# Kernel tuning notes

Hardware: AMD Instinct MI355X
Metric: run time of the kernel (lower is better)

## Reference

```python
import jax, jax.numpy as jnp
import numpy as np

VOCAB, EMB, H, TRK, L, BOUND = 50257, 1024, 1024, 1024, 256, 25

def setup_inputs() -> dict:
    key = jax.random.key(0)
    ks = jax.random.split(key, 16)
    s = 0.02
    return {
        "query_words": jax.random.normal(ks[0], (L, 1, H), jnp.float32),
        "query_vector": jax.random.normal(ks[1], (1, 1, TRK), jnp.float32),
        "decision_vector": jax.random.normal(ks[2], (1, 1, H), jnp.float32),
        "target_answer": jax.random.randint(ks[3], (BOUND, 1, 1), 0, VOCAB, jnp.int64),
        "emb_table": jax.random.normal(ks[4], (VOCAB, EMB), jnp.float32) * s,
        "gru_Wih": jax.random.normal(ks[5], (3 * H, EMB + TRK), jnp.float32) * s,
        "gru_Whh": jax.random.normal(ks[6], (3 * H, H), jnp.float32) * s,
        "gru_bih": jnp.zeros((3 * H,), jnp.float32),
        "gru_bhh": jnp.zeros((3 * H,), jnp.float32),
        "attn_Wq": jax.random.normal(ks[7], (H, H), jnp.float32) * s,
        "attn_bq": jnp.zeros((H,), jnp.float32),
        "attn_Wk": jax.random.normal(ks[8], (H, H), jnp.float32) * s,
        "attn_bk": jnp.zeros((H,), jnp.float32),
        "attn_v": jax.random.normal(ks[9], (H,), jnp.float32) * s,
        "concat_W": jax.random.normal(ks[10], (H, 2 * H), jnp.float32) * s,
        "concat_b": jnp.zeros((H,), jnp.float32),
        "out_W": jax.random.normal(ks[11], (VOCAB, H), jnp.float32) * s,
        "out_b": jnp.zeros((VOCAB,), jnp.float32),
    }


def reference(query_words, query_vector, decision_vector, target_answer,
              emb_table, gru_Wih, gru_Whh, gru_bih, gru_bhh,
              attn_Wq, attn_bq, attn_Wk, attn_bk, attn_v,
              concat_W, concat_b, out_W, out_b):
    # eval-mode: dropout = identity; tf_ratio=1 -> teacher forcing for all steps
    h_dim = decision_vector.shape[-1]
    qw = query_words[:, 0, :]                      # [L, H] encoder memory
    keys = qw @ attn_Wk.T + attn_bk                # precompute key projection once
    qv = query_vector.reshape(-1)                  # [TRK]
    h0 = decision_vector.reshape(-1)               # [H]
    ta = target_answer.reshape(-1).astype(jnp.int32)
    # input token per step: SOS (0), then teacher-forced targets
    idx_seq = jnp.concatenate([jnp.zeros((1,), jnp.int32), ta[: BOUND - 1]])

    def step(h, idx):
        x = jnp.concatenate([qv, emb_table[idx]])  # cat(query_vector, embedded)
        g = gru_Wih @ x + gru_bih                  # [3H]
        gh = gru_Whh @ h + gru_bhh                 # [3H]
        r = jax.nn.sigmoid(g[:h_dim] + gh[:h_dim])
        z = jax.nn.sigmoid(g[h_dim:2 * h_dim] + gh[h_dim:2 * h_dim])
        n = jnp.tanh(g[2 * h_dim:] + r * gh[2 * h_dim:])
        h_new = (1.0 - z) * n + z * h
        # additive (Bahdanau) attention over query_words
        e = jnp.tanh(keys + attn_Wq @ h_new + attn_bq) @ attn_v  # [L]
        w = jax.nn.softmax(e)
        ctx = w @ qw                                              # [H]
        vec = jnp.tanh(concat_W @ jnp.concatenate([h_new, ctx]) + concat_b)
        logits = out_W @ vec + out_b                              # [VOCAB]
        return h_new, jax.nn.log_softmax(logits)

    _, logps = jax.lax.scan(step, h0, idx_seq)     # [BOUND, VOCAB]
    answer = jnp.argmax(logps, axis=-1)            # greedy tokens per step
    return (answer, logps)
```

## Files before the change

### kernel.cpp

```cpp
#include <hip/hip_runtime.h>
#include <math.h>

#define VOCAB 50257
#define EMB 1024
#define HD 1024
#define TRK 1024
#define LQ 256
#define BND 25
#define SENT 0xAAAAAAAAu

__device__ __forceinline__ float wred(float s){
  #pragma unroll
  for (int m = 32; m >= 1; m >>= 1) s += __shfl_xor(s, m, 64);
  return s;
}

__global__ __launch_bounds__(256) void k_pre_keys(const float* __restrict__ Wih,
                                                  const float* __restrict__ qv,
                                                  const float* __restrict__ bih,
                                                  const int*   __restrict__ ta,
                                                  const float* __restrict__ emb,
                                                  const float* __restrict__ qw,
                                                  const float* __restrict__ Wk,
                                                  float* __restrict__ gib,
                                                  float* __restrict__ E,
                                                  float* __restrict__ part){
  __shared__ float qt[64*256];
  int b = blockIdx.x, tid = threadIdx.x;
  if (b < 768){
    int w = tid >> 6, lane = tid & 63;
    int row = b*4 + w;
    const float* a = Wih + (size_t)row*2048;
    float s = 0.f;
    #pragma unroll
    for (int e = 0; e < 4; e++){
      int k = e*256 + lane*4;
      float4 av = *(const float4*)(a + k);
      float4 qr = *(const float4*)(qv + k);
      s += av.x*qr.x + av.y*qr.y + av.z*qr.z + av.w*qr.w;
    }
    s = wred(s);
    if (lane == 0) gib[row] = s + bih[row];
    return;
  }
  if (b < 868){
    int g = (b - 768)*256 + tid;
    int t = g >> 10, i = g & 1023;
    int idx = (t == 0) ? 0 : ta[t-1];
    E[g] = emb[(size_t)idx*EMB + i];
    return;
  }
  int b2 = b - 868;
  int jb = b2 & 63;
  int ks = b2 >> 6;
  int l = tid;
  float acc[16];
  #pragma unroll
  for (int j = 0; j < 16; j++) acc[j] = 0.f;

  for (int kt = 0; kt < 4; kt++){
    int kb = ks*256 + kt*64;
    __syncthreads();
    #pragma unroll
    for (int p = 0; p < 16; p++){
      int fidx = (p*256 + tid)*4;
      int kk = fidx & 63, ll = fidx >> 6;
      float4 v = *(const float4*)(qw + (size_t)ll*1024 + kb + kk);
      qt[(kk+0)*256 + (ll ^ ((kk+0)&31))] = v.x;
      qt[(kk+1)*256 + (ll ^ ((kk+1)&31))] = v.y;
      qt[(kk+2)*256 + (ll ^ ((kk+2)&31))] = v.z;
      qt[(kk+3)*256 + (ll ^ ((kk+3)&31))] = v.w;
    }
    __syncthreads();
    #pragma unroll
    for (int s = 0; s < 4; s++){
      float qr[16];
      #pragma unroll
      for (int q = 0; q < 16; q++){
        int k = s*16 + q;
        qr[q] = qt[k*256 + (l ^ (k&31))];
      }
      #pragma unroll
      for (int j = 0; j < 16; j++){
        const float* wr = Wk + (size_t)(jb*16 + j)*1024 + kb + s*16;
        #pragma unroll
        for (int q4 = 0; q4 < 4; q4++){
          float4 wv = *(const float4*)(wr + q4*4);
          acc[j] += qr[q4*4+0]*wv.x + qr[q4*4+1]*wv.y
                  + qr[q4*4+2]*wv.z + qr[q4*4+3]*wv.w;
        }
      }
    }
  }
  #pragma unroll
  for (int j = 0; j < 16; j++)
    part[((size_t)ks*1024 + jb*16 + j)*256 + l] = acc[j];
}

template<int K, int NCH>
__global__ __launch_bounds__(256) void k_gemm_s2(const float* __restrict__ A, int lda,
                                                 const float* __restrict__ B, int ldb,
                                                 const float* __restrict__ bias,
                                                 float* __restrict__ C,
                                                 int R, int N, int act){
  __shared__ float Bl[NCH*K];
  constexpr int KD4 = K/4;
  int tid = threadIdx.x, w = tid >> 6, lane = tid & 63;
  int row = blockIdx.x*4 + w;
  const float* a = A + (size_t)row*lda;
  float4 ar[K/256];
  #pragma unroll
  for (int e = 0; e < K/256; e++)
    ar[e] = *(const float4*)(a + e*256 + lane*4);
  float bs = bias[row];
  for (int c0 = 0; c0 < N; c0 += NCH){
    int nt = min(NCH, N - c0);
    __syncthreads();
    int total = nt*KD4;
    for (int i = tid; i < total; i += 256){
      int j = i/KD4, kk = i - j*KD4;
      *(float4*)&Bl[j*K + kk*4] = *(const float4*)(B + (size_t)(c0+j)*ldb + kk*4);
    }
    __syncthreads();
    for (int j = 0; j < nt; j++){
      float s = 0.f;
      #pragma unroll
      for (int e = 0; e < K/256; e++){
        float4 bv = *(const float4*)&Bl[j*K + e*256 + lane*4];
        s += ar[e].x*bv.x + ar[e].y*bv.y + ar[e].z*bv.z + ar[e].w*bv.w;
      }
      s = wred(s);
      if (lane == 0){
        float v = s + bs;
        if (act) v = tanhf(v);
        C[(size_t)(c0+j)*R + row] = v;
      }
    }
  }
}

__global__ __launch_bounds__(512, 1) void k_gru8(const float* __restrict__ Whh,
                                                 const float* __restrict__ bhh,
                                                 const float* __restrict__ gi,
                                                 const float* __restrict__ dv,
                                                 float* __restrict__ HC,
                                                 unsigned* __restrict__ hxu){
  __shared__ float Wl[24][1024];
  __shared__ float hbuf[1024];
  __shared__ float sres[24];
  int tid = threadIdx.x, w = tid >> 6, lane = tid & 63;
  int b = blockIdx.x;
  for (int i = tid; i < 6144; i += 512){
    int r = i >> 8, c = (i & 255)*4;
    int g = r >> 3, s = r & 7;
    *(float4*)&Wl[r][c] = *(const float4*)(Whh + (size_t)(g*1024 + b*8 + s)*1024 + c);
  }
  if (tid < 256)
    *(float4*)&hbuf[tid*4] = *(const float4*)(dv + tid*4);
  __syncthreads();

  for (int t = 0; t < BND; t++){
    float g0=0,g1=0,g2=0,bb0=0,bb1=0,bb2=0,hpown=0;
    if (tid < 8){
      int i = b*8 + tid;
      const float* gg = gi + (size_t)t*3072;
      g0 = gg[i]; g1 = gg[1024+i]; g2 = gg[2048+i];
      bb0 = bhh[i]; bb1 = bhh[1024+i]; bb2 = bhh[2048+i];
      hpown = hbuf[i];
    }
    float hv[16];
    #pragma unroll
    for (int e = 0; e < 4; e++){
      float4 v = *(const float4*)&hbuf[e*256 + lane*4];
      hv[e*4]=v.x; hv[e*4+1]=v.y; hv[e*4+2]=v.z; hv[e*4+3]=v.w;
    }
    #pragma unroll
    for (int j = 0; j < 3; j++){
      int r = w*3 + j;
      float a = 0.f;
      #pragma unroll
      for (int e = 0; e < 4; e++){
        float4 v = *(const float4*)&Wl[r][e*256 + lane*4];
        a += v.x*hv[e*4] + v.y*hv[e*4+1] + v.z*hv[e*4+2] + v.w*hv[e*4+3];
      }
      a = wred(a);
      if (lane == 0) sres[r] = a;
    }
    __syncthreads();
    if (tid < 8){
      int i = b*8 + tid;
      float ghr = sres[tid]      + bb0;
      float ghz = sres[8  + tid] + bb1;
      float ghn = sres[16 + tid] + bb2;
      float rr = 1.f/(1.f + expf(-(g0 + ghr)));
      float zz = 1.f/(1.f + expf(-(g1 + ghz)));
      float nn = tanhf(g2 + rr*ghn);
      float hnew = (1.f - zz)*nn + zz*hpown;
      HC[(size_t)t*2048 + i] = hnew;
      if (t < BND-1){
        union { float f; unsigned u; } cv; cv.f = hnew;
        if (cv.u == SENT) cv.u ^= 1u;
        __hip_atomic_store(hxu + (size_t)t*2048 + b*16 + tid, cv.u,
                           __ATOMIC_RELAXED, __HIP_MEMORY_SCOPE_AGENT);
      }
    }
    if (t == BND-1) break;
    if (w < 2){
      int blk = w*64 + lane;
      const unsigned* bp = hxu + (size_t)t*2048 + blk*16;
      unsigned d[8];
      for (;;){
        bool ok = true;
        #pragma unroll
        for (int j = 0; j < 8; j++){
          d[j] = __hip_atomic_load(bp + j, __ATOMIC_RELAXED, __HIP_MEMORY_SCOPE_AGENT);
          ok = ok && (d[j] != SENT);
        }
        if (ok) break;
        __builtin_amdgcn_s_sleep(1);
      }
      #pragma unroll
      for (int j = 0; j < 8; j++)
        hbuf[blk*8 + j] = __uint_as_float(d[j]);
    }
    __syncthreads();
  }
}

__global__ __launch_bounds__(256) void k_attn1(const float* __restrict__ part,
                                               const float* __restrict__ bk,
                                               const float* __restrict__ Qt,
                                               const float* __restrict__ av,
                                               float* __restrict__ epart){
  int t = blockIdx.x, jc = blockIdx.y;
  int l = threadIdx.x;
  const float* q = Qt + (size_t)t*1024;
  int j0 = jc*32;
  float acc = 0.f;
  #pragma unroll
  for (int u = 0; u < 8; u++){
    #pragma unroll
    for (int v = 0; v < 4; v++){
      int j = j0 + u*4 + v;
      float kv = part[(size_t)j*256 + l]
               + part[(size_t)(1024+j)*256 + l]
               + part[(size_t)(2048+j)*256 + l]
               + part[(size_t)(3072+j)*256 + l]
               + bk[j];
      acc += tanhf(kv + q[j]) * av[j];
    }
  }
  epart[((size_t)t*32 + jc)*256 + l] = acc;
}

__global__ __launch_bounds__(256) void k_attn2(const float* __restrict__ epart,
                                               const float* __restrict__ qw,
                                               float* __restrict__ HC){
  __shared__ float red[256];
  __shared__ float sw[256];
  int t = blockIdx.x, tid = threadIdx.x;
  float e = 0.f;
  for (int jc = 0; jc < 32; jc++) e += epart[((size_t)t*32 + jc)*256 + tid];
  red[tid] = e; __syncthreads();
  for (int s = 128; s > 0; s >>= 1){
    if (tid < s) red[tid] = fmaxf(red[tid], red[tid+s]);
    __syncthreads();
  }
  float m = red[0]; __syncthreads();
  float wv = expf(e - m);
  red[tid] = wv; __syncthreads();
  for (int s = 128; s > 0; s >>= 1){
    if (tid < s) red[tid] += red[tid+s];
    __syncthreads();
  }
  float inv = 1.f/red[0];
  sw[tid] = wv*inv; __syncthreads();
  float4 c = make_float4(0.f,0.f,0.f,0.f);
  const float* qp = qw + tid*4;
  for (int ll = 0; ll < 256; ll++){
    float wl = sw[ll];
    float4 v = *(const float4*)(qp + (size_t)ll*1024);
    c.x += wl*v.x; c.y += wl*v.y; c.z += wl*v.z; c.w += wl*v.w;
  }
  *(float4*)(HC + (size_t)t*2048 + 1024 + tid*4) = c;
}

__global__ __launch_bounds__(256, 1) void k_gemm_big9(const float* __restrict__ A,
                                                      const float* __restrict__ B,
                                                      const float* __restrict__ bias,
                                                      float* __restrict__ C){
  __shared__ float Bl[25600];
  int tid = threadIdx.x;
  int rl = tid & 63;
  int q  = tid >> 6;
  int R0 = blockIdx.x*256;

  for (int i = tid; i < 6400; i += 256){
    int t = i >> 8, kk = (i & 255) << 2;
    *(float4*)&Bl[t*1024 + kk] = *(const float4*)(B + (size_t)t*1024 + kk);
  }

  const float* ap[4];
  #pragma unroll
  for (int j = 0; j < 4; j++){
    int r = R0 + 64*j + rl;
    if (r >= VOCAB) r = VOCAB-1;
    ap[j] = A + (size_t)r*1024 + q*256;
  }

  float acc[4][25];
  #pragma unroll
  for (int j = 0; j < 4; j++)
    #pragma unroll
    for (int t = 0; t < 25; t++) acc[j][t] = 0.f;

  float4 a[4][4];
  #pragma unroll
  for (int j = 0; j < 4; j++){
    a[j][0] = *(const float4*)(ap[j] + 0);
    a[j][1] = *(const float4*)(ap[j] + 4);
    a[j][2] = *(const float4*)(ap[j] + 8);
    a[j][3] = *(const float4*)(ap[j] + 12);
  }
  __syncthreads();

  const float* bq = Bl + q*256;
  #pragma unroll 1
  for (int kb = 0; kb < 256; kb += 16){
    float4 n[4][4];
    if (kb + 16 < 256){
      #pragma unroll
      for (int j = 0; j < 4; j++){
        n[j][0] = *(const float4*)(ap[j] + kb + 16);
        n[j][1] = *(const float4*)(ap[j] + kb + 20);
        n[j][2] = *(const float4*)(ap[j] + kb + 24);
        n[j][3] = *(const float4*)(ap[j] + kb + 28);
      }
    }
    #pragma unroll
    for (int t = 0; t < 25; t++){
      const float* bt = bq + t*1024 + kb;
      float4 b0 = *(const float4*)(bt + 0);
      float4 b1 = *(const float4*)(bt + 4);
      float4 b2 = *(const float4*)(bt + 8);
      float4 b3 = *(const float4*)(bt + 12);
      #pragma unroll
      for (int j = 0; j < 4; j++){
        acc[j][t] += a[j][0].x*b0.x + a[j][0].y*b0.y + a[j][0].z*b0.z + a[j][0].w*b0.w
                   + a[j][1].x*b1.x + a[j][1].y*b1.y + a[j][1].z*b1.z + a[j][1].w*b1.w
                   + a[j][2].x*b2.x + a[j][2].y*b2.y + a[j][2].z*b2.z + a[j][2].w*b2.w
                   + a[j][3].x*b3.x + a[j][3].y*b3.y + a[j][3].z*b3.z + a[j][3].w*b3.w;
      }
    }
    #pragma unroll
    for (int j = 0; j < 4; j++){
      a[j][0] = n[j][0]; a[j][1] = n[j][1]; a[j][2] = n[j][2]; a[j][3] = n[j][3];
    }
  }

  for (int tc0 = 0; tc0 < 25; tc0 += 13){
    int nt = min(13, 25 - tc0);
    __syncthreads();
    #pragma unroll
    for (int j = 0; j < 4; j++)
      for (int tt = 0; tt < nt; tt++)
        Bl[(q*256 + j*64 + rl)*13 + tt] = acc[j][tc0 + tt];
    __syncthreads();
    for (int v = tid; v < 256*nt; v += 256){
      int rr = v & 255, tt = v >> 8;
      float s = 0.f;
      #pragma unroll
      for (int qq = 0; qq < 4; qq++)
        s += Bl[(qq*256 + rr)*13 + tt];
      int row = R0 + rr;
      if (row < VOCAB)
        C[(size_t)(tc0 + tt)*VOCAB + row] = s + bias[row];
    }
  }
}

__global__ __launch_bounds__(256) void k_lstat(const float* __restrict__ C,
                                               float* __restrict__ pm,
                                               float* __restrict__ ps,
                                               int*   __restrict__ pa){
  __shared__ float sm[256], ss[256];
  __shared__ int   sa[256];
  int t = blockIdx.x, c = blockIdx.y, tid = threadIdx.x;
  int r0 = c*6283, r1 = min(r0 + 6283, VOCAB);
  const float* p = C + (size_t)t*VOCAB;
  float m = -3.4e38f, s = 0.f; int arg = r0;
  for (int r = r0 + tid; r < r1; r += 256){
    float x = p[r];
    if (x > m){ s = s*expf(m - x) + 1.f; m = x; arg = r; }
    else       s += expf(x - m);
  }
  sm[tid] = m; ss[tid] = s; sa[tid] = arg; __syncthreads();
  for (int st = 128; st > 0; st >>= 1){
    if (tid < st){
      float m1 = sm[tid], s1 = ss[tid]; int a1 = sa[tid];
      float m2 = sm[tid+st], s2 = ss[tid+st]; int a2 = sa[tid+st];
      if (m2 > m1){ sm[tid] = m2; ss[tid] = s2 + s1*expf(m1 - m2); sa[tid] = a2; }
      else if (m2 == m1){ ss[tid] = s1 + s2; sa[tid] = min(a1, a2); }
      else { ss[tid] = s1 + s2*expf(m2 - m1); }
    }
    __syncthreads();
  }
  if (tid == 0){ pm[t*8 + c] = sm[0]; ps[t*8 + c] = ss[0]; pa[t*8 + c] = sa[0]; }
}

__global__ __launch_bounds__(256) void k_lsub2(float* __restrict__ C,
                                               const float* __restrict__ pm,
                                               const float* __restrict__ ps,
                                               const int* __restrict__ pa,
                                               float* __restrict__ out){
  int t = blockIdx.y;
  float M = pm[t*8], S = ps[t*8]; int A = pa[t*8];
  #pragma unroll
  for (int c = 1; c < 8; c++){
    float m2 = pm[t*8+c], s2 = ps[t*8+c]; int a2 = pa[t*8+c];
    if (m2 > M){ S = s2 + S*expf(M - m2); M = m2; A = a2; }
    else if (m2 == M){ S += s2; A = min(A, a2); }
    else S += s2*expf(m2 - M);
  }
  float Lg = logf(S) + M;
  int r = blockIdx.x*256 + threadIdx.x;
  if (r < VOCAB) C[(size_t)t*VOCAB + r] -= Lg;
  if (blockIdx.x == 0 && threadIdx.x == 0) out[t] = (float)A;
}

extern "C" void kernel_launch(void* const* d_in, const int* in_sizes, int n_in,
                              void* d_out, int out_size, void* d_ws, size_t ws_size,
                              hipStream_t stream){
  const float* qw  = (const float*)d_in[0];
  const float* qv  = (const float*)d_in[1];
  const float* dv  = (const float*)d_in[2];
  const int*   ta  = (const int*)d_in[3];
  const float* emb = (const float*)d_in[4];
  const float* Wih = (const float*)d_in[5];
  const float* Whh = (const float*)d_in[6];
  const float* bih = (const float*)d_in[7];
  const float* bhh = (const float*)d_in[8];
  const float* Wq  = (const float*)d_in[9];
  const float* bq  = (const float*)d_in[10];
  const float* Wk  = (const float*)d_in[11];
  const float* bk  = (const float*)d_in[12];
  const float* av  = (const float*)d_in[13];
  const float* cW  = (const float*)d_in[14];
  const float* cb  = (const float*)d_in[15];
  const float* oW  = (const float*)d_in[16];
  const float* ob  = (const float*)d_in[17];
  float* out = (float*)d_out;
  float* ws  = (float*)d_ws;

  float* part  = ws;
  float* ep    = ws + 1048576;
  float* E     = ws + 1310720;
  float* gib   = ws + 1336320;
  float* gi    = ws + 1339392;
  float* HC    = ws + 1416192;
  float* Qt    = ws + 1467392;
  float* VEC   = ws + 1492992;
  unsigned* hx = (unsigned*)(ws + 1518592);
  float* pm    = ws + 1569792;
  float* ps    = ws + 1570048;
  int*   pa    = (int*)(ws + 1570304);

  hipMemsetAsync(hx, 0xAA, 51200*4, stream);
  k_pre_keys<<<1124, 256, 0, stream>>>(Wih, qv, bih, ta, emb, qw, Wk, gib, E, part);
  k_gemm_s2<1024,16><<<768, 256, 0, stream>>>(Wih + 1024, 2048, E, 1024, gib, gi, 3072, 25, 0);
  k_gru8<<<128, 512, 0, stream>>>(Whh, bhh, gi, dv, HC, hx);
  k_gemm_s2<1024,16><<<256, 256, 0, stream>>>(Wq, 1024, HC, 2048, bq, Qt, 1024, 25, 0);
  k_attn1<<<dim3(25,32), 256, 0, stream>>>(part, bk, Qt, av, ep);
  k_attn2<<<25, 256, 0, stream>>>(ep, qw, HC);
  k_gemm_s2<2048,8><<<256, 256, 0, stream>>>(cW, 2048, HC, 2048, cb, VEC, 1024, 25, 1);
  k_gemm_big9<<<197, 256, 0, stream>>>(oW, VEC, ob, out + 25);
  k_lstat<<<dim3(25,8), 256, 0, stream>>>(out + 25, pm, ps, pa);
  k_lsub2<<<dim3(197,25), 256, 0, stream>>>(out + 25, pm, ps, pa, out);
}
```

Baseline: 396.0 us.

## Compute output projection with split-bf16 MFMA instead of FP32 FMA

Replaces the FP32 FMA output-vocabulary GEMM with a matrix-core kernel. Both operands are split into bf16 high and low parts, and three MFMA products (hi*hi, hi*lo, lo*hi) approximate FP32 accuracy. A small new kernel pre-splits the 25 decoder vectors, while the weight rows are split on the fly in registers. The aim is to shorten the largest GEMM (50257x1024x25), at the cost of conversion ALU work, an extra launch and slightly reduced precision.

```diff
diff --git a/kernel.cpp b/kernel.cpp
--- a/kernel.cpp
+++ b/kernel.cpp
@@ -8,6 +8,9 @@
 #define LQ 256
 #define BND 25
 #define SENT 0xAAAAAAAAu
+
+typedef __attribute__((ext_vector_type(8))) short short8v;
+typedef __attribute__((ext_vector_type(4))) float float4v;
 
 __device__ __forceinline__ float wred(float s){
   #pragma unroll
@@ -285,96 +288,92 @@
   *(float4*)(HC + (size_t)t*2048 + 1024 + tid*4) = c;
 }
 
-__global__ __launch_bounds__(256, 1) void k_gemm_big9(const float* __restrict__ A,
-                                                      const float* __restrict__ B,
+__global__ __launch_bounds__(256) void k_bconv(const float* __restrict__ VEC,
+                                               short* __restrict__ Bhi,
+                                               short* __restrict__ Blo){
+  int i = blockIdx.x*256 + threadIdx.x;
+  if (i < 25600){
+    float v = VEC[i];
+    unsigned bits = __float_as_uint(v);
+    unsigned hib = bits & 0xFFFF0000u;
+    Bhi[i] = (short)(bits >> 16);
+    float lo = v - __uint_as_float(hib);
+    Blo[i] = (short)(__float_as_uint(lo) >> 16);
+  }
+}
+
+__global__ __launch_bounds__(256, 1) void k_gemm_mfma(const float* __restrict__ A,
+                                                      const short* __restrict__ Bhi,
+                                                      const short* __restrict__ Blo,
                                                       const float* __restrict__ bias,
                                                       float* __restrict__ C){
-  __shared__ float Bl[25600];
-  int tid = threadIdx.x;
-  int rl = tid & 63;
-  int q  = tid >> 6;
-  int R0 = blockIdx.x*256;
-
-  for (int i = tid; i < 6400; i += 256){
-    int t = i >> 8, kk = (i & 255) << 2;
-    *(float4*)&Bl[t*1024 + kk] = *(const float4*)(B + (size_t)t*1024 + kk);
-  }
+  int tid = threadIdx.x, lane = tid & 63, w = tid >> 6;
+  int rlo = lane & 15, kg = lane >> 4;
+  int R0 = blockIdx.x*256 + w*64;
 
   const float* ap[4];
   #pragma unroll
-  for (int j = 0; j < 4; j++){
-    int r = R0 + 64*j + rl;
-    if (r >= VOCAB) r = VOCAB-1;
-    ap[j] = A + (size_t)r*1024 + q*256;
-  }
-
-  float acc[4][25];
-  #pragma unroll
-  for (int j = 0; j < 4; j++)
-    #pragma unroll
-    for (int t = 0; t < 25; t++) acc[j][t] = 0.f;
-
-  float4 a[4][4];
-  #pragma unroll
-  for (int j = 0; j < 4; j++){
-    a[j][0] = *(const float4*)(ap[j] + 0);
-    a[j][1] = *(const float4*)(ap[j] + 4);
-    a[j][2] = *(const float4*)(ap[j] + 8);
-    a[j][3] = *(const float4*)(ap[j] + 12);
-  }
-  __syncthreads();
-
-  const float* bq = Bl + q*256;
+  for (int rt = 0; rt < 4; rt++){
+    int row = R0 + rt*16 + rlo;
+    if (row >= VOCAB) row = VOCAB-1;
+    ap[rt] = A + (size_t)row*1024 + kg*8;
+  }
+  int t0 = rlo;
+  int t1 = 16 + rlo; if (t1 > 24) t1 = 24;
+  const short* bh0 = Bhi + t0*1024 + kg*8;
+  const short* bl0 = Blo + t0*1024 + kg*8;
+  const short* bh1 = Bhi + t1*1024 + kg*8;
+  const short* bl1 = Blo + t1*1024 + kg*8;
+
+  float4v acc[4][2];
+  #pragma unroll
+  for (int rt = 0; rt < 4; rt++)
+    #pragma unroll
+    for (int ct = 0; ct < 2; ct++)
+      acc[rt][ct] = (float4v){0.f,0.f,0.f,0.f};
+
   #pragma unroll 1
-  for (int kb = 0; kb < 256; kb += 16){
-    float4 n[4][4];
-    if (kb + 16 < 256){
-      #pragma unroll
-      for (int j = 0; j < 4; j++){
-        n[j][0] = *(const float4*)(ap[j] + kb + 16);
-        n[j][1] = *(const float4*)(ap[j] + kb + 20);
-        n[j][2] = *(const float4*)(ap[j] + kb + 24);
-        n[j][3] = *(const float4*)(ap[j] + kb + 28);
-      }
-    }
-    #pragma unroll
-    for (int t = 0; t < 25; t++){
-      const float* bt = bq + t*1024 + kb;
-      float4 b0 = *(const float4*)(bt + 0);
-      float4 b1 = *(const float4*)(bt + 4);
-      float4 b2 = *(const float4*)(bt + 8);
-      float4 b3 = *(const float4*)(bt + 12);
-      #pragma unroll
-      for (int j = 0; j < 4; j++){
-        acc[j][t] += a[j][0].x*b0.x + a[j][0].y*b0.y + a[j][0].z*b0.z + a[j][0].w*b0.w
-                   + a[j][1].x*b1.x + a[j][1].y*b1.y + a[j][1].z*b1.z + a[j][1].w*b1.w
-                   + a[j][2].x*b2.x + a[j][2].y*b2.y + a[j][2].z*b2.z + a[j][2].w*b2.w
-                   + a[j][3].x*b3.x + a[j][3].y*b3.y + a[j][3].z*b3.z + a[j][3].w*b3.w;
-      }
-    }
-    #pragma unroll
-    for (int j = 0; j < 4; j++){
-      a[j][0] = n[j][0]; a[j][1] = n[j][1]; a[j][2] = n[j][2]; a[j][3] = n[j][3];
-    }
-  }
-
-  for (int tc0 = 0; tc0 < 25; tc0 += 13){
-    int nt = min(13, 25 - tc0);
-    __syncthreads();
-    #pragma unroll
-    for (int j = 0; j < 4; j++)
-      for (int tt = 0; tt < nt; tt++)
-        Bl[(q*256 + j*64 + rl)*13 + tt] = acc[j][tc0 + tt];
-    __syncthreads();
-    for (int v = tid; v < 256*nt; v += 256){
-      int rr = v & 255, tt = v >> 8;
-      float s = 0.f;
-      #pragma unroll
-      for (int qq = 0; qq < 4; qq++)
-        s += Bl[(qq*256 + rr)*13 + tt];
-      int row = R0 + rr;
-      if (row < VOCAB)
-        C[(size_t)(tc0 + tt)*VOCAB + row] = s + bias[row];
+  for (int s = 0; s < 32; s++){
+    int ko = s*32;
+    short8v bh[2], bl[2];
+    bh[0] = *(const short8v*)(bh0 + ko);
+    bl[0] = *(const short8v*)(bl0 + ko);
+    bh[1] = *(const short8v*)(bh1 + ko);
+    bl[1] = *(const short8v*)(bl1 + ko);
+    #pragma unroll
+    for (int rt = 0; rt < 4; rt++){
+      float4 a0 = *(const float4*)(ap[rt] + ko);
+      float4 a1 = *(const float4*)(ap[rt] + ko + 4);
+      float av[8] = {a0.x,a0.y,a0.z,a0.w,a1.x,a1.y,a1.z,a1.w};
+      short8v ah, al;
+      #pragma unroll
+      for (int j = 0; j < 8; j++){
+        unsigned bits = __float_as_uint(av[j]);
+        ah[j] = (short)(bits >> 16);
+        float lo = av[j] - __uint_as_float(bits & 0xFFFF0000u);
+        al[j] = (short)(__float_as_uint(lo) >> 16);
+      }
+      #pragma unroll
+      for (int ct = 0; ct < 2; ct++){
+        acc[rt][ct] = __builtin_amdgcn_mfma_f32_16x16x32_bf16(ah, bh[ct], acc[rt][ct], 0, 0, 0);
+        acc[rt][ct] = __builtin_amdgcn_mfma_f32_16x16x32_bf16(ah, bl[ct], acc[rt][ct], 0, 0, 0);
+        acc[rt][ct] = __builtin_amdgcn_mfma_f32_16x16x32_bf16(al, bh[ct], acc[rt][ct], 0, 0, 0);
+      }
+    }
+  }
+
+  #pragma unroll
+  for (int rt = 0; rt < 4; rt++){
+    #pragma unroll
+    for (int ct = 0; ct < 2; ct++){
+      int t = ct*16 + rlo;
+      if (t >= 25) continue;
+      #pragma unroll
+      for (int reg = 0; reg < 4; reg++){
+        int row = R0 + rt*16 + kg*4 + reg;
+        if (row < VOCAB)
+          C[(size_t)t*VOCAB + row] = acc[rt][ct][reg] + bias[row];
+      }
     }
   }
 }
@@ -464,6 +463,8 @@
   float* pm    = ws + 1569792;
   float* ps    = ws + 1570048;
   int*   pa    = (int*)(ws + 1570304);
+  short* Bhi   = (short*)(ws + 1570816);
+  short* Blo   = (short*)(ws + 1583616);
 
   hipMemsetAsync(hx, 0xAA, 51200*4, stream);
   k_pre_keys<<<1124, 256, 0, stream>>>(Wih, qv, bih, ta, emb, qw, Wk, gib, E, part);
@@ -473,7 +474,8 @@
   k_attn1<<<dim3(25,32), 256, 0, stream>>>(part, bk, Qt, av, ep);
   k_attn2<<<25, 256, 0, stream>>>(ep, qw, HC);
   k_gemm_s2<2048,8><<<256, 256, 0, stream>>>(cW, 2048, HC, 2048, cb, VEC, 1024, 25, 1);
-  k_gemm_big9<<<197, 256, 0, stream>>>(oW, VEC, ob, out + 25);
+  k_bconv<<<100, 256, 0, stream>>>(VEC, Bhi, Blo);
+  k_gemm_mfma<<<197, 256, 0, stream>>>(oW, Bhi, Blo, ob, out + 25);
   k_lstat<<<dim3(25,8), 256, 0, stream>>>(out + 25, pm, ps, pa);
   k_lsub2<<<dim3(197,25), 256, 0, stream>>>(out + 25, pm, ps, pa, out);
 }
```

Result: faster. 375.2 us (-5.3%).
